# Optimization experiments

Hardware: AMD Instinct MI355X
Metric: run time of the kernel (lower is better)

Reference implementation:

```python
import jax, jax.numpy as jnp
import numpy as np

NDIM = 128
GDIM = 128
NUM_LAYERS = 2
B = 8192
IDX = 16          # nodes per graph
EPG = 32          # edges per graph
N = B * IDX       # total nodes = 131072
E = B * EPG       # total edges = 262144


def setup_inputs() -> dict:
    key = jax.random.key(0)
    ks = jax.random.split(key, 24)
    h = jax.random.normal(ks[0], (B, IDX, NDIM), dtype=jnp.float32)
    # edges constrained within each graph (flattened node indexing)
    gid = jnp.repeat(jnp.arange(B, dtype=jnp.int64), EPG)
    src = gid * IDX + jax.random.randint(ks[1], (E,), 0, IDX).astype(jnp.int64)
    dst = gid * IDX + jax.random.randint(ks[2], (E,), 0, IDX).astype(jnp.int64)
    edge_index = jnp.stack([src, dst], axis=0)
    s = 0.05
    inp = {
        'h': h,
        'edge_index': edge_index,
        'msg_W': jax.random.normal(ks[3], (NUM_LAYERS, 2 * NDIM, 2 * NDIM), jnp.float32) * s,
        'msg_b': jax.random.normal(ks[4], (NUM_LAYERS, 2 * NDIM), jnp.float32) * s,
        'msgr_W': jax.random.normal(ks[5], (NUM_LAYERS, 2 * NDIM, 2 * NDIM), jnp.float32) * s,
        'msgr_b': jax.random.normal(ks[6], (NUM_LAYERS, 2 * NDIM), jnp.float32) * s,
        'gru_Wih': jax.random.normal(ks[7], (NUM_LAYERS, 3 * NDIM, 2 * NDIM), jnp.float32) * s,
        'gru_Whh': jax.random.normal(ks[8], (NUM_LAYERS, 3 * NDIM, NDIM), jnp.float32) * s,
        'gru_bih': jax.random.normal(ks[9], (NUM_LAYERS, 3 * NDIM), jnp.float32) * s,
        'gru_bhh': jax.random.normal(ks[10], (NUM_LAYERS, 3 * NDIM), jnp.float32) * s,
        'fm_W': jax.random.normal(ks[11], (GDIM, NDIM), jnp.float32) * s,
        'fm_b': jax.random.normal(ks[12], (GDIM,), jnp.float32) * s,
        'gm_W': jax.random.normal(ks[13], (1, NDIM), jnp.float32) * s,
        'gm_b': jax.random.normal(ks[14], (1,), jnp.float32) * s,
        'fmi_W': jax.random.normal(ks[15], (GDIM, NDIM), jnp.float32) * s,
        'fmi_b': jax.random.normal(ks[16], (GDIM,), jnp.float32) * s,
        'gmi_W': jax.random.normal(ks[17], (1, NDIM), jnp.float32) * s,
        'gmi_b': jax.random.normal(ks[18], (1,), jnp.float32) * s,
    }
    return inp


def _gnn_forward(h, edge_index, msg_W, msg_b, msgr_W, msgr_b,
                 gru_Wih, gru_Whh, gru_bih, gru_bhh):
    # h: [N, ndim]; edge_index: [2, E] -> doubled with reversed edges -> [2, 2E]
    ei = jnp.concatenate([edge_index, edge_index[::-1]], axis=1)
    src, dst = ei[0], ei[1]
    e = edge_index.shape[1]
    n_nodes = h.shape[0]
    for l in range(NUM_LAYERS):
        # (eval mode: dropout p=0.0 is a no-op)
        h_j = h[src]                       # [2E, ndim]
        h_i = h[dst]                       # [2E, ndim]
        m = jnp.concatenate([h_j, h_i], axis=1)   # [2E, 2*ndim]
        m_fwd, m_rev = m[:e], m[e:]
        a = jnp.concatenate([
            m_fwd @ msg_W[l].T + msg_b[l],
            m_rev @ msgr_W[l].T + msgr_b[l],
        ], axis=0)                          # [2E, 2*ndim]
        aggr = jax.ops.segment_sum(a, dst, num_segments=n_nodes)  # [N, 2*ndim]
        # GRUCell(aggr, h): gate order r, z, n (torch convention)
        gi = aggr @ gru_Wih[l].T + gru_bih[l]   # [N, 3*ndim]
        gh = h @ gru_Whh[l].T + gru_bhh[l]      # [N, 3*ndim]
        gi_r, gi_z, gi_n = jnp.split(gi, 3, axis=1)
        gh_r, gh_z, gh_n = jnp.split(gh, 3, axis=1)
        r = jax.nn.sigmoid(gi_r + gh_r)
        z = jax.nn.sigmoid(gi_z + gh_z)
        n = jnp.tanh(gi_n + r * gh_n)
        h = n + z * (h - n)                 # (1-z)*n + z*h
    return h


def _graph_aggr(h, idx, f_W, f_b, g_W, g_b):
    # gated sum aggregation
    h_vG = h @ f_W.T + f_b                      # [N, gdim]
    g_vG = jax.nn.sigmoid(h @ g_W.T + g_b)      # [N, 1]
    out = (h_vG * g_vG).reshape(-1, idx, f_W.shape[0])
    return out.sum(axis=1)                      # [B, gdim]


def reference(h, edge_index, msg_W, msg_b, msgr_W, msgr_b,
              gru_Wih, gru_Whh, gru_bih, gru_bhh,
              fm_W, fm_b, gm_W, gm_b, fmi_W, fmi_b, gmi_W, gmi_b):
    idx = h.shape[1]
    hf = h.reshape(-1, NDIM)
    hf = _gnn_forward(hf, edge_index, msg_W, msg_b, msgr_W, msgr_b,
                      gru_Wih, gru_Whh, gru_bih, gru_bhh)
    h_G = _graph_aggr(hf, idx, fm_W, fm_b, gm_W, gm_b)
    h_G_init = _graph_aggr(hf, idx, fmi_W, fmi_b, gmi_W, gmi_b)
    return (hf.reshape(-1, idx, NDIM), h_G, h_G_init)
```

## Files before the change

kernel.cpp:

```cpp
#include <hip/hip_runtime.h>
#include <math.h>
#include <stdint.h>

#define NDIM 128
#define B_GRAPHS 8192
#define IDX 16
#define EPG 32
#define NN (B_GRAPHS*IDX)
#define NE (B_GRAPHS*EPG)

typedef short bf16x8 __attribute__((ext_vector_type(8)));
typedef float f32x4  __attribute__((ext_vector_type(4)));

__device__ inline unsigned short f2bf(float x) {
    union { float f; unsigned u; } v; v.f = x;
    unsigned r = v.u + 0x7fff + ((v.u >> 16) & 1);
    return (unsigned short)(r >> 16);
}
__device__ inline float bf2f(unsigned short b) {
    union { unsigned u; float f; } v; v.u = ((unsigned)b) << 16;
    return v.f;
}
__device__ inline float sigm(float x) { return 1.f/(1.f + __expf(-x)); }
__device__ inline float tanh_f(float x) {
    float ax = fabsf(x);
    float t  = __expf(-2.f*ax);
    float r  = (1.f - t)/(1.f + t);
    return copysignf(r, x);
}

#define GLOAD_LDS16(g, l) \
    __builtin_amdgcn_global_load_lds( \
        (const __attribute__((address_space(1))) unsigned int*)(g), \
        (__attribute__((address_space(3))) unsigned int*)(l), 16, 0, 0)

__global__ __launch_bounds__(256) void composemm_kernel(
    const float* __restrict__ msg_W, const float* __restrict__ msgr_W,
    const float* __restrict__ Wih, unsigned short* __restrict__ WB)
{
    int bid = blockIdx.x;
    int l  = bid / 48; int rem = bid - l*48;
    int ct = rem >> 3, kt = rem & 7;
    const int t = threadIdx.x;
    __shared__ float Ws[64][33];
    __shared__ float Ms[32][65];
    const float* wih    = Wih   + (size_t)l*384*256;
    const float* msgWl  = msg_W + (size_t)l*256*256;
    const float* msgrWl = msgr_W+ (size_t)l*256*256;
    float acc[4][4] = {};
    const int tr  = (t >> 4) * 4;
    const int tcc = (t & 15) * 4;
    for (int q0 = 0; q0 < 256; q0 += 32) {
#pragma unroll
        for (int i = 0; i < 8; i++) {
            int u = i*256 + t; int r = u >> 5, q = u & 31;
            Ws[r][q] = wih[(size_t)(ct*64 + r)*256 + q0 + q];
        }
#pragma unroll
        for (int i = 0; i < 8; i++) {
            int u = i*256 + t; int q = u >> 6, c = u & 63;
            int kk = kt*64 + c;
            int piece = kk >> 7;
            const float* M = (piece & 1) ? msgrWl : msgWl;
            int sc = (kk & 127) + ((piece >> 1) << 7);
            Ms[q][c] = M[(size_t)(q0 + q)*256 + sc];
        }
        __syncthreads();
#pragma unroll 8
        for (int q = 0; q < 32; q++) {
#pragma unroll
            for (int i2 = 0; i2 < 4; i2++) {
                float wv = Ws[tr + i2][q];
#pragma unroll
                for (int j2 = 0; j2 < 4; j2++)
                    acc[i2][j2] = fmaf(wv, Ms[q][tcc + j2], acc[i2][j2]);
            }
        }
        __syncthreads();
    }
#pragma unroll
    for (int i2 = 0; i2 < 4; i2++) {
        int cold = ct*64 + tr + i2;
        int cc = cold & 127, t2 = cold >> 7;
        int colp = ((cc >> 4) << 6) + (t2 << 4) + (cc & 15);
#pragma unroll
        for (int j2 = 0; j2 < 4; j2++) {
            int k = kt*64 + tcc + j2;
            WB[(size_t)l*512*640 + (size_t)colp*640 + k] = f2bf(acc[i2][j2]);
        }
    }
}

__global__ __launch_bounds__(256) void compose_kernel(
    const float* __restrict__ msg_W, const float* __restrict__ msgr_W,
    const float* __restrict__ Wih,   const float* __restrict__ Whh,
    const float* __restrict__ msg_b, const float* __restrict__ msgr_b,
    unsigned short* __restrict__ WB, float* __restrict__ c34)
{
    int idx = blockIdx.x*256 + threadIdx.x;
    const int TWB = 2*512*640;
    if (idx < TWB) {
        int l = idx / (512*640); int rem = idx - l*(512*640);
        int cold = rem / 640; int k = rem - cold*640;
        float val;
        if (k < 512) {
            if (cold < 384) return;
            val = 0.f;
        } else {
            int kk = k - 512;
            if (cold < 256)      val = Whh[l*384*128 + cold*128 + kk];
            else if (cold < 384) val = 0.f;
            else                 val = Whh[l*384*128 + (cold-128)*128 + kk];
        }
        int cc = cold & 127, t = cold >> 7;
        int colp = ((cc >> 4) << 6) + (t << 4) + (cc & 15);
        WB[l*512*640 + colp*640 + k] = f2bf(val);
    } else if (idx < TWB + 2*2*384) {
        int i2 = idx - TWB;
        int l = i2 / 768; int rem = i2 - l*768;
        int which = rem / 384; int r = rem - which*384;
        const float* wih = Wih + l*384*256 + r*256;
        const float* bb  = (which ? msgr_b : msg_b) + l*256;
        float acc = 0.f;
        for (int q = 0; q < 256; q++) acc = fmaf(wih[q], bb[q], acc);
        c34[l*768 + which*384 + r] = acc;
    }
}

__global__ __launch_bounds__(128) void init_kernel(
    const float* __restrict__ hin, const int* __restrict__ ei,
    unsigned short* __restrict__ A, float* __restrict__ indeg,
    float* __restrict__ outdeg, unsigned char* __restrict__ pack)
{
    int g = blockIdx.x, t = threadIdx.x;
    __shared__ float hb[16][128];
    __shared__ float sin_[16][128];
    __shared__ float sout_[16][128];
    __shared__ int sl[32], dl[32];
    __shared__ int cin[16], cout[16];
    __shared__ int flag64;
    int base = g*IDX;
    for (int r = 0; r < 16; r++) hb[r][t] = hin[(size_t)(base+r)*128 + t];
    for (int r = 0; r < 16; r++) { sin_[r][t] = 0.f; sout_[r][t] = 0.f; }
    if (t < 16) { cin[t] = 0; cout[t] = 0; }
    if (t == 0) {
        int orv = 0;
        for (int i = 1; i < 64; i += 2) orv |= ei[i];
        flag64 = (orv == 0);
    }
    __syncthreads();
    if (t < 32) {
        int e = g*EPG + t;
        int sv, dv;
        if (flag64) { sv = ei[2*e]; dv = ei[2*(NE + e)]; }
        else        { sv = ei[e];   dv = ei[NE + e];     }
        sl[t] = sv - base; dl[t] = dv - base;
        atomicAdd(&cout[sl[t]], 1); atomicAdd(&cin[dl[t]], 1);
        pack[g*32 + t] = (unsigned char)((sl[t] & 15) | ((dl[t] & 15) << 4));
    }
    __syncthreads();
    for (int e = 0; e < 32; e++) {
        sin_[dl[e]][t]  += hb[sl[e]][t];
        sout_[sl[e]][t] += hb[dl[e]][t];
    }
    __syncthreads();
    {
        size_t gbase = (size_t)base * 640;
#pragma unroll
        for (int i = 0; i < 10; i++) {
            int u = i*128 + t;
            int row = u / 80;
            int j   = u - row*80;
            int seg = j >> 4;
            int c0  = (j & 15) * 8;
            float vals[8];
            if (seg == 0) {
#pragma unroll
                for (int k2 = 0; k2 < 8; k2++) vals[k2] = sin_[row][c0+k2];
            } else if (seg == 1) {
#pragma unroll
                for (int k2 = 0; k2 < 8; k2++) vals[k2] = sout_[row][c0+k2];
            } else {
                float s = (seg == 2) ? (float)cin[row]
                        : (seg == 3) ? (float)cout[row] : 1.f;
#pragma unroll
                for (int k2 = 0; k2 < 8; k2++) vals[k2] = hb[row][c0+k2] * s;
            }
            bf16x8 w;
#pragma unroll
            for (int k2 = 0; k2 < 8; k2++) w[k2] = (short)f2bf(vals[k2]);
            *(bf16x8*)(A + gbase + (size_t)row*640 + seg*128 + c0) = w;
        }
    }
    if (t < 16) { indeg[base+t] = (float)cin[t]; outdeg[base+t] = (float)cout[t]; }
}

struct FSmem {
    unsigned short As[2][64*64];
    union {
        unsigned short Bs[2][384*32];
        unsigned short hnewB[64*128];
    } u;
    unsigned char csr[4][2][17];
    unsigned char adj[4][2][32];
    unsigned char offj[4][2][16];
    float gates[2][64];
};

#define MF(a,b,c) __builtin_amdgcn_mfma_f32_16x16x32_bf16((a),(b),(c),0,0,0)

#define CSTEP(BB, AB, E, J2) do {                                             \
    const unsigned short* Asb = sm.As[AB];                                    \
    const unsigned short* Bsb = sm.u.Bs[BB];                                  \
    bf16x8 bfv[3];                                                            \
    _Pragma("unroll")                                                         \
    for (int tt = 0; tt < 3; tt++) {                                          \
        int a0 = wid*48 + tt*16 + l15;                                        \
        bfv[tt] = *(const bf16x8*)(Bsb + a0*32 + (l4 ^ ((a0>>1)&3))*8);       \
    }                                                                         \
    bf16x8 afv[4];                                                            \
    _Pragma("unroll")                                                         \
    for (int mi = 0; mi < 4; mi++) {                                          \
        int row = mi*16 + l15;                                                \
        int slot = ((E)*4 + l4) ^ (row & 7);                                  \
        afv[mi] = *(const bf16x8*)(Asb + row*64 + slot*8);                    \
    }                                                                         \
    __builtin_amdgcn_s_setprio(1);                                            \
    _Pragma("unroll")                                                         \
    for (int mi = 0; mi < 4; mi++) {                                          \
        acc[mi][0]  = MF(afv[mi], bfv[0], acc[mi][0]);                        \
        acc[mi][1]  = MF(afv[mi], bfv[1], acc[mi][1]);                        \
        acc[mi][J2] = MF(afv[mi], bfv[2], acc[mi][J2]);                       \
    }                                                                         \
    __builtin_amdgcn_s_setprio(0);                                            \
} while (0)

#define WB0 asm volatile("s_waitcnt vmcnt(0)\n\ts_barrier" ::: "memory")
#define WB1 asm volatile("s_waitcnt vmcnt(1)\n\ts_barrier" ::: "memory")

template <bool FINAL>
__global__ __launch_bounds__(512, 4) void fused_kernel(
    unsigned short* __restrict__ A,
    const unsigned short* __restrict__ WBl,
    const unsigned char* __restrict__ pack,
    const float* __restrict__ c34l,
    const float* __restrict__ bihl, const float* __restrict__ bhhl,
    const float* __restrict__ gmW,  const float* __restrict__ gmb,
    const float* __restrict__ gmiW, const float* __restrict__ gmib,
    float* __restrict__ hf, float* __restrict__ P1, float* __restrict__ P2,
    float* __restrict__ sg)
{
    __shared__ FSmem sm;
    const int n0  = blockIdx.x * 64;
    const int g0  = blockIdx.x * 4;
    const int tid = threadIdx.x;
    const int lane = tid & 63, wid = tid >> 6;
    const int l15 = lane & 15, l4 = lane >> 4;

    const int arow = tid >> 3;
    const unsigned short* Abase =
        A + (size_t)(n0 + arow)*640 + (size_t)(((tid & 7) ^ (arow & 7)) * 8);
    int boffv[3], baddv[3];
#pragma unroll
    for (int i = 0; i < 3; i++) {
        int u = i*512 + tid;
        int a = u >> 2, s = u & 3;
        int grp = a / 48, rem = a - grp*48;
        int tt = rem >> 4, clo = rem & 15;
        boffv[i] = (grp*64 + tt*16 + clo)*640 + (s ^ ((a >> 1) & 3))*8;
        baddv[i] = (tt == 2) ? 16*640 : 0;
    }

    auto STAGE_A2 = [&](int p) {
        GLOAD_LDS16(Abase + p*64, sm.As[p & 1] + tid*8);
    };
    auto STAGE_B = [&](int kst) {
        unsigned short* dst = sm.u.Bs[kst & 1] + tid*8;
        const unsigned short* srcb = WBl + kst*32;
        if (kst < 16) {
#pragma unroll
            for (int i = 0; i < 3; i++)
                GLOAD_LDS16(srcb + boffv[i], dst + i*4096);
        } else {
#pragma unroll
            for (int i = 0; i < 3; i++)
                GLOAD_LDS16(srcb + boffv[i] + baddv[i], dst + i*4096);
        }
    };

    STAGE_B(0); STAGE_A2(0);
    if (tid < 8) {
        int gl = tid >> 1, dir = tid & 1;
        const unsigned char* pk = pack + (size_t)(g0 + gl)*32;
        unsigned char* C = sm.csr[gl][dir];
        for (int d = 0; d < 17; d++) C[d] = 0;
        for (int e = 0; e < 32; e++) {
            int p = pk[e];
            int key = dir ? (p & 15) : (p >> 4);
            C[key + 1]++;
        }
        for (int d = 0; d < 16; d++) { C[d+1] += C[d]; sm.offj[gl][dir][d] = C[d]; }
        for (int e = 0; e < 32; e++) {
            int p = pk[e];
            int key = dir ? (p & 15) : (p >> 4);
            int val = dir ? (p >> 4) : (p & 15);
            sm.adj[gl][dir][sm.offj[gl][dir][key]++] = val;
        }
    }

    f32x4 acc[4][4] = {};

    WB0;
    STAGE_B(1);  STAGE_A2(1); CSTEP(0, 0, 0, 2);
    WB1; STAGE_B(2);          CSTEP(1, 0, 1, 2);
    WB0; STAGE_B(3);  STAGE_A2(2); CSTEP(0, 1, 0, 2);
    WB1; STAGE_B(4);          CSTEP(1, 1, 1, 2);
    WB0; STAGE_B(5);  STAGE_A2(3); CSTEP(0, 0, 0, 2);
    WB1; STAGE_B(6);          CSTEP(1, 0, 1, 2);
    WB0; STAGE_B(7);  STAGE_A2(4); CSTEP(0, 1, 0, 2);
    WB1; STAGE_B(8);          CSTEP(1, 1, 1, 2);
    WB0; STAGE_B(9);  STAGE_A2(5); CSTEP(0, 0, 0, 2);
    WB1; STAGE_B(10);         CSTEP(1, 0, 1, 2);
    WB0; STAGE_B(11); STAGE_A2(6); CSTEP(0, 1, 0, 2);
    WB1; STAGE_B(12);         CSTEP(1, 1, 1, 2);
    WB0; STAGE_B(13); STAGE_A2(7); CSTEP(0, 0, 0, 2);
    WB1; STAGE_B(14);         CSTEP(1, 0, 1, 2);
    WB0; STAGE_B(15); STAGE_A2(8); CSTEP(0, 1, 0, 2);
    WB1; STAGE_B(16);         CSTEP(1, 1, 1, 2);
    WB0; STAGE_B(17); STAGE_A2(9); CSTEP(0, 0, 0, 3);
    WB1; STAGE_B(18);         CSTEP(1, 0, 1, 3);
    WB0; STAGE_B(19);         CSTEP(0, 1, 0, 3);
    WB0;                      CSTEP(1, 1, 1, 3);

    {
        const int chn = wid*16 + l15;
        const unsigned short* Ah = (chn < 64) ? sm.As[0] : sm.As[1];
        const int kl = chn & 63;
        const int klo = ((kl >> 3) << 3);
        float c3r = c34l[chn],     c3z = c34l[128+chn], c3n = c34l[256+chn];
        float c4r = c34l[384+chn], c4z = c34l[512+chn], c4n = c34l[640+chn];
        float br   = bihl[chn]     + bhhl[chn];
        float bz   = bihl[128+chn] + bhhl[128+chn];
        float bin_ = bihl[256+chn];
        float bhn_ = bhhl[256+chn];
#pragma unroll
        for (int mi = 0; mi < 4; mi++) {
#pragma unroll
            for (int q = 0; q < 4; q++) {
                int row = mi*16 + l4*4 + q;
                size_t v = (size_t)n0 + row;
                int gl = row >> 4, d = row & 15;
                float di  = (float)(sm.csr[gl][0][d+1] - sm.csr[gl][0][d]);
                float dof = (float)(sm.csr[gl][1][d+1] - sm.csr[gl][1][d]);
                float hold = bf2f(Ah[row*64 + (((kl>>3) ^ (row&7))<<3) + (kl&7)]);
                float rr = sigm(acc[mi][0][q] + di*c3r + dof*c4r + br);
                float zz = sigm(acc[mi][1][q] + di*c3z + dof*c4z + bz);
                float nn = tanh_f(acc[mi][2][q] + di*c3n + dof*c4n + bin_
                                  + rr*(acc[mi][3][q] + bhn_));
                float hv = nn + zz*(hold - nn);
                *(unsigned short*)((char*)sm.u.hnewB
                    + row*256 + ((((chn>>3) ^ (row&7))<<4) + ((chn&7)<<1))) = f2bf(hv);
                if (FINAL) hf[v*128 + chn] = hv;
            }
        }
    }
    __syncthreads();

    if (!FINAL) {
#pragma unroll
        for (int i = 0; i < 10; i++) {
            int u   = i*512 + tid;
            int seg = u >> 10;
            int row = (u >> 4) & 63;
            int c8  = u & 15;
            int gl = row >> 4, d = row & 15;
            float out8[8];
            if (seg < 2) {
#pragma unroll
                for (int k = 0; k < 8; k++) out8[k] = 0.f;
                int e0 = sm.csr[gl][seg][d], e1 = sm.csr[gl][seg][d+1];
                int rb = gl*16;
                for (int j = e0; j < e1; j++) {
                    int r2 = rb + sm.adj[gl][seg][j];
                    bf16x8 v8 = *(const bf16x8*)((const char*)sm.u.hnewB
                                 + r2*256 + ((c8 ^ (r2 & 7)) << 4));
#pragma unroll
                    for (int k = 0; k < 8; k++)
                        out8[k] += bf2f((unsigned short)v8[k]);
                }
            } else {
                bf16x8 v8 = *(const bf16x8*)((const char*)sm.u.hnewB
                             + row*256 + ((c8 ^ (row & 7)) << 4));
                float sc = 1.f;
                if (seg == 2)
                    sc = (float)(sm.csr[gl][0][d+1] - sm.csr[gl][0][d]);
                else if (seg == 3)
                    sc = (float)(sm.csr[gl][1][d+1] - sm.csr[gl][1][d]);
#pragma unroll
                for (int k = 0; k < 8; k++)
                    out8[k] = bf2f((unsigned short)v8[k]) * sc;
            }
            bf16x8 w;
#pragma unroll
            for (int k = 0; k < 8; k++) w[k] = (short)f2bf(out8[k]);
            *(bf16x8*)(A + (size_t)(n0 + row)*640 + seg*128 + c8*8) = w;
        }
    } else {
        if (tid < 64) {
            int row = tid;
            float a1 = 0.f, a2 = 0.f;
            for (int s = 0; s < 16; s++) {
                bf16x8 hv8 = *(const bf16x8*)((const char*)sm.u.hnewB
                              + row*256 + ((s ^ (row & 7)) << 4));
#pragma unroll
                for (int j = 0; j < 8; j++) {
                    float x = bf2f((unsigned short)hv8[j]);
                    int c = s*8 + j;
                    a1 = fmaf(gmW[c],  x, a1);
                    a2 = fmaf(gmiW[c], x, a2);
                }
            }
            sm.gates[0][row] = sigm(a1 + gmb[0]);
            sm.gates[1][row] = sigm(a2 + gmib[0]);
        }
        __syncthreads();
        int c = tid & 127, gq = tid >> 7;
        int rb = gq*16;
        float p1 = 0.f, p2 = 0.f;
        for (int r = 0; r < 16; r++) {
            int rr = rb + r;
            float x = bf2f(*(const unsigned short*)((const char*)sm.u.hnewB
                           + rr*256 + ((((c>>3) ^ (rr&7))<<4) + ((c&7)<<1))));
            p1 = fmaf(sm.gates[0][rr], x, p1);
            p2 = fmaf(sm.gates[1][rr], x, p2);
        }
        size_t g = g0 + gq;
        P1[g*128 + c] = p1;
        P2[g*128 + c] = p2;
        if (tid < 8) {
            int gl = tid >> 1, w = tid & 1;
            float s = 0.f;
            for (int r = 0; r < 16; r++) s += sm.gates[w][gl*16 + r];
            sg[(size_t)(g0 + gl)*2 + w] = s;
        }
    }
}

__global__ __launch_bounds__(256) void outgemm_kernel(
    const float* __restrict__ P1, const float* __restrict__ P2,
    const float* __restrict__ sg,
    const float* __restrict__ fm_W,  const float* __restrict__ fm_b,
    const float* __restrict__ fmi_W, const float* __restrict__ fmi_b,
    float* __restrict__ out1, float* __restrict__ out2)
{
    const int g0 = blockIdx.x * 32;
    const int t  = threadIdx.x;
    __shared__ float Ws[128][33];
    __shared__ float Ps[32][33];
    const int tc = t & 15, tg = t >> 4;

    for (int pass = 0; pass < 2; pass++) {
        const float* P  = pass ? P2 : P1;
        const float* W  = pass ? fmi_W : fm_W;
        const float* bb = pass ? fmi_b : fm_b;
        float acc[2][8] = {};
        for (int kc = 0; kc < 128; kc += 32) {
#pragma unroll
            for (int i = 0; i < 16; i++) {
                int u = i*256 + t; int r = u >> 5, k = u & 31;
                Ws[r][k] = W[(size_t)r*128 + kc + k];
            }
#pragma unroll
            for (int i = 0; i < 4; i++) {
                int u = i*256 + t; int r = u >> 5, k = u & 31;
                Ps[r][k] = P[(size_t)(g0 + r)*128 + kc + k];
            }
            __syncthreads();
#pragma unroll 8
            for (int k = 0; k < 32; k++) {
                float p0 = Ps[tg*2][k], p1v = Ps[tg*2+1][k];
#pragma unroll
                for (int j = 0; j < 8; j++) {
                    float w = Ws[tc*8+j][k];
                    acc[0][j] = fmaf(p0,  w, acc[0][j]);
                    acc[1][j] = fmaf(p1v, w, acc[1][j]);
                }
            }
            __syncthreads();
        }
        float* outp = pass ? out2 : out1;
#pragma unroll
        for (int i = 0; i < 2; i++) {
            int g = g0 + tg*2 + i;
            float sgv = sg[g*2 + pass];
#pragma unroll
            for (int j = 0; j < 8; j++) {
                int cc = tc*8 + j;
                outp[(size_t)g*128 + cc] = acc[i][j] + bb[cc]*sgv;
            }
        }
    }
}

extern "C" void kernel_launch(void* const* d_in, const int* in_sizes, int n_in,
                              void* d_out, int out_size, void* d_ws, size_t ws_size,
                              hipStream_t stream)
{
    const float* h     = (const float*)d_in[0];
    const int*   ei    = (const int*)d_in[1];
    const float* msgW  = (const float*)d_in[2];
    const float* msgb  = (const float*)d_in[3];
    const float* msgrW = (const float*)d_in[4];
    const float* msgrb = (const float*)d_in[5];
    const float* Wih   = (const float*)d_in[6];
    const float* Whh   = (const float*)d_in[7];
    const float* bih   = (const float*)d_in[8];
    const float* bhh   = (const float*)d_in[9];
    const float* fmW   = (const float*)d_in[10];
    const float* fmb   = (const float*)d_in[11];
    const float* gmW   = (const float*)d_in[12];
    const float* gmb   = (const float*)d_in[13];
    const float* fmiW  = (const float*)d_in[14];
    const float* fmib  = (const float*)d_in[15];
    const float* gmiW  = (const float*)d_in[16];
    const float* gmib  = (const float*)d_in[17];

    char* w = (char*)d_ws;
    unsigned short* A    = (unsigned short*)w;  w += (size_t)NN*640*2;
    unsigned short* WB   = (unsigned short*)w;  w += (size_t)2*512*640*2;
    float* c34   = (float*)w;                   w += (size_t)2*768*4;
    float* indeg = (float*)w;                   w += (size_t)NN*4;
    float* outdeg= (float*)w;                   w += (size_t)NN*4;
    unsigned char* pack = (unsigned char*)w;    w += (size_t)B_GRAPHS*32;
    float* P1    = (float*)w;                   w += (size_t)B_GRAPHS*128*4;
    float* P2    = (float*)w;                   w += (size_t)B_GRAPHS*128*4;
    float* sgb   = (float*)w;                   w += (size_t)B_GRAPHS*2*4;

    float* hf   = (float*)d_out;
    float* out1 = hf + (size_t)NN*128;
    float* out2 = out1 + (size_t)B_GRAPHS*128;

    composemm_kernel<<<96, 256, 0, stream>>>(msgW, msgrW, Wih, WB);
    int compose_items = 2*512*640 + 2*2*384;
    compose_kernel<<<(compose_items + 255)/256, 256, 0, stream>>>(
        msgW, msgrW, Wih, Whh, msgb, msgrb, WB, c34);

    init_kernel<<<B_GRAPHS, 128, 0, stream>>>(h, ei, A, indeg, outdeg, pack);

    fused_kernel<false><<<NN/64, 512, 0, stream>>>(
        A, WB, pack, c34, bih, bhh,
        gmW, gmb, gmiW, gmib, nullptr, nullptr, nullptr, nullptr);
    fused_kernel<true><<<NN/64, 512, 0, stream>>>(
        A, WB + (size_t)512*640, pack,
        c34 + 768, bih + 384, bhh + 384,
        gmW, gmb, gmiW, gmib, hf, P1, P2, sgb);

    outgemm_kernel<<<B_GRAPHS/32, 256, 0, stream>>>(
        P1, P2, sgb, fmW, fmb, fmiW, fmib, out1, out2);
}
```

Before: 412.3 us.

## Fuse both GNN layers into one kernel launch with block-local feature rewrite

Merges the two per-layer fused kernel launches into a single kernel that runs both layers back to back in each block. Each block rewrites its own A rows between layers, followed by a vmcnt wait and a barrier, and skips the separate CSR rebuild and launch. This works because edges stay inside a graph and a block owns whole graphs. It also drops the unused indeg/outdeg writes from init. The cost is that the second layer's A reads go back through global memory/L2 right after this block's own writes, which relies on intra-block visibility, and there are no cross-kernel boundaries left to hide latency.

After: 494.4 us. 19.9% more time.

```diff
diff --git a/kernel.cpp b/kernel.cpp
--- a/kernel.cpp
+++ b/kernel.cpp
@@ -129,8 +129,7 @@
 
 __global__ __launch_bounds__(128) void init_kernel(
     const float* __restrict__ hin, const int* __restrict__ ei,
-    unsigned short* __restrict__ A, float* __restrict__ indeg,
-    float* __restrict__ outdeg, unsigned char* __restrict__ pack)
+    unsigned short* __restrict__ A, unsigned char* __restrict__ pack)
 {
     int g = blockIdx.x, t = threadIdx.x;
     __shared__ float hb[16][128];
@@ -192,7 +191,6 @@
             *(bf16x8*)(A + gbase + (size_t)row*640 + seg*128 + c0) = w;
         }
     }
-    if (t < 16) { indeg[base+t] = (float)cin[t]; outdeg[base+t] = (float)cout[t]; }
 }
 
 struct FSmem {
@@ -238,13 +236,12 @@
 #define WB0 asm volatile("s_waitcnt vmcnt(0)\n\ts_barrier" ::: "memory")
 #define WB1 asm volatile("s_waitcnt vmcnt(1)\n\ts_barrier" ::: "memory")
 
-template <bool FINAL>
-__global__ __launch_bounds__(512, 4) void fused_kernel(
+__global__ __launch_bounds__(512, 4) void gnn_kernel(
     unsigned short* __restrict__ A,
-    const unsigned short* __restrict__ WBl,
+    const unsigned short* __restrict__ WB,
     const unsigned char* __restrict__ pack,
-    const float* __restrict__ c34l,
-    const float* __restrict__ bihl, const float* __restrict__ bhhl,
+    const float* __restrict__ c34,
+    const float* __restrict__ bih, const float* __restrict__ bhh,
     const float* __restrict__ gmW,  const float* __restrict__ gmb,
     const float* __restrict__ gmiW, const float* __restrict__ gmib,
     float* __restrict__ hf, float* __restrict__ P1, float* __restrict__ P2,
@@ -258,7 +255,7 @@
     const int l15 = lane & 15, l4 = lane >> 4;
 
     const int arow = tid >> 3;
-    const unsigned short* Abase =
+    unsigned short* Abase =
         A + (size_t)(n0 + arow)*640 + (size_t)(((tid & 7) ^ (arow & 7)) * 8);
     int boffv[3], baddv[3];
 #pragma unroll
@@ -271,24 +268,6 @@
         baddv[i] = (tt == 2) ? 16*640 : 0;
     }
 
-    auto STAGE_A2 = [&](int p) {
-        GLOAD_LDS16(Abase + p*64, sm.As[p & 1] + tid*8);
-    };
-    auto STAGE_B = [&](int kst) {
-        unsigned short* dst = sm.u.Bs[kst & 1] + tid*8;
-        const unsigned short* srcb = WBl + kst*32;
-        if (kst < 16) {
-#pragma unroll
-            for (int i = 0; i < 3; i++)
-                GLOAD_LDS16(srcb + boffv[i], dst + i*4096);
-        } else {
-#pragma unroll
-            for (int i = 0; i < 3; i++)
-                GLOAD_LDS16(srcb + boffv[i] + baddv[i], dst + i*4096);
-        }
-    };
-
-    STAGE_B(0); STAGE_A2(0);
     if (tid < 8) {
         int gl = tid >> 1, dir = tid & 1;
         const unsigned char* pk = pack + (size_t)(g0 + gl)*32;
@@ -308,122 +287,149 @@
         }
     }
 
-    f32x4 acc[4][4] = {};
-
-    WB0;
-    STAGE_B(1);  STAGE_A2(1); CSTEP(0, 0, 0, 2);
-    WB1; STAGE_B(2);          CSTEP(1, 0, 1, 2);
-    WB0; STAGE_B(3);  STAGE_A2(2); CSTEP(0, 1, 0, 2);
-    WB1; STAGE_B(4);          CSTEP(1, 1, 1, 2);
-    WB0; STAGE_B(5);  STAGE_A2(3); CSTEP(0, 0, 0, 2);
-    WB1; STAGE_B(6);          CSTEP(1, 0, 1, 2);
-    WB0; STAGE_B(7);  STAGE_A2(4); CSTEP(0, 1, 0, 2);
-    WB1; STAGE_B(8);          CSTEP(1, 1, 1, 2);
-    WB0; STAGE_B(9);  STAGE_A2(5); CSTEP(0, 0, 0, 2);
-    WB1; STAGE_B(10);         CSTEP(1, 0, 1, 2);
-    WB0; STAGE_B(11); STAGE_A2(6); CSTEP(0, 1, 0, 2);
-    WB1; STAGE_B(12);         CSTEP(1, 1, 1, 2);
-    WB0; STAGE_B(13); STAGE_A2(7); CSTEP(0, 0, 0, 2);
-    WB1; STAGE_B(14);         CSTEP(1, 0, 1, 2);
-    WB0; STAGE_B(15); STAGE_A2(8); CSTEP(0, 1, 0, 2);
-    WB1; STAGE_B(16);         CSTEP(1, 1, 1, 2);
-    WB0; STAGE_B(17); STAGE_A2(9); CSTEP(0, 0, 0, 3);
-    WB1; STAGE_B(18);         CSTEP(1, 0, 1, 3);
-    WB0; STAGE_B(19);         CSTEP(0, 1, 0, 3);
-    WB0;                      CSTEP(1, 1, 1, 3);
-
+    auto do_layer = [&](const unsigned short* WBl, const float* c34l,
+                        const float* bihl, const float* bhhl, bool fin) {
+        auto STAGE_A2 = [&](int p) {
+            GLOAD_LDS16(Abase + p*64, sm.As[p & 1] + tid*8);
+        };
+        auto STAGE_B = [&](int kst) {
+            unsigned short* dst = sm.u.Bs[kst & 1] + tid*8;
+            const unsigned short* srcb = WBl + kst*32;
+            if (kst < 16) {
+#pragma unroll
+                for (int i = 0; i < 3; i++)
+                    GLOAD_LDS16(srcb + boffv[i], dst + i*4096);
+            } else {
+#pragma unroll
+                for (int i = 0; i < 3; i++)
+                    GLOAD_LDS16(srcb + boffv[i] + baddv[i], dst + i*4096);
+            }
+        };
+
+        f32x4 acc[4][4] = {};
+
+        STAGE_B(0); STAGE_A2(0);
+        WB0;
+        STAGE_B(1);  STAGE_A2(1); CSTEP(0, 0, 0, 2);
+        WB1; STAGE_B(2);          CSTEP(1, 0, 1, 2);
+        WB0; STAGE_B(3);  STAGE_A2(2); CSTEP(0, 1, 0, 2);
+        WB1; STAGE_B(4);          CSTEP(1, 1, 1, 2);
+        WB0; STAGE_B(5);  STAGE_A2(3); CSTEP(0, 0, 0, 2);
+        WB1; STAGE_B(6);          CSTEP(1, 0, 1, 2);
+        WB0; STAGE_B(7);  STAGE_A2(4); CSTEP(0, 1, 0, 2);
+        WB1; STAGE_B(8);          CSTEP(1, 1, 1, 2);
+        WB0; STAGE_B(9);  STAGE_A2(5); CSTEP(0, 0, 0, 2);
+        WB1; STAGE_B(10);         CSTEP(1, 0, 1, 2);
+        WB0; STAGE_B(11); STAGE_A2(6); CSTEP(0, 1, 0, 2);
+        WB1; STAGE_B(12);         CSTEP(1, 1, 1, 2);
+        WB0; STAGE_B(13); STAGE_A2(7); CSTEP(0, 0, 0, 2);
+        WB1; STAGE_B(14);         CSTEP(1, 0, 1, 2);
+        WB0; STAGE_B(15); STAGE_A2(8); CSTEP(0, 1, 0, 2);
+        WB1; STAGE_B(16);         CSTEP(1, 1, 1, 2);
+        WB0; STAGE_B(17); STAGE_A2(9); CSTEP(0, 0, 0, 3);
+        WB1; STAGE_B(18);         CSTEP(1, 0, 1, 3);
+        WB0; STAGE_B(19);         CSTEP(0, 1, 0, 3);
+        WB0;                      CSTEP(1, 1, 1, 3);
+
+        {
+            const int chn = wid*16 + l15;
+            const unsigned short* Ah = (chn < 64) ? sm.As[0] : sm.As[1];
+            const int kl = chn & 63;
+            float c3r = c34l[chn],     c3z = c34l[128+chn], c3n = c34l[256+chn];
+            float c4r = c34l[384+chn], c4z = c34l[512+chn], c4n = c34l[640+chn];
+            float br   = bihl[chn]     + bhhl[chn];
+            float bz   = bihl[128+chn] + bhhl[128+chn];
+            float bin_ = bihl[256+chn];
+            float bhn_ = bhhl[256+chn];
+#pragma unroll
+            for (int mi = 0; mi < 4; mi++) {
+#pragma unroll
+                for (int q = 0; q < 4; q++) {
+                    int row = mi*16 + l4*4 + q;
+                    size_t v = (size_t)n0 + row;
+                    int gl = row >> 4, d = row & 15;
+                    float di  = (float)(sm.csr[gl][0][d+1] - sm.csr[gl][0][d]);
+                    float dof = (float)(sm.csr[gl][1][d+1] - sm.csr[gl][1][d]);
+                    float hold = bf2f(Ah[row*64 + (((kl>>3) ^ (row&7))<<3) + (kl&7)]);
+                    float rr = sigm(acc[mi][0][q] + di*c3r + dof*c4r + br);
+                    float zz = sigm(acc[mi][1][q] + di*c3z + dof*c4z + bz);
+                    float nn = tanh_f(acc[mi][2][q] + di*c3n + dof*c4n + bin_
+                                      + rr*(acc[mi][3][q] + bhn_));
+                    float hv = nn + zz*(hold - nn);
+                    *(unsigned short*)((char*)sm.u.hnewB
+                        + row*256 + ((((chn>>3) ^ (row&7))<<4) + ((chn&7)<<1))) = f2bf(hv);
+                    if (fin) hf[v*128 + chn] = hv;
+                }
+            }
+        }
+        __syncthreads();
+
+        if (!fin) {
+#pragma unroll
+            for (int i = 0; i < 10; i++) {
+                int u   = i*512 + tid;
+                int seg = u >> 10;
+                int row = (u >> 4) & 63;
+                int c8  = u & 15;
+                int gl = row >> 4, d = row & 15;
+                float out8[8];
+                if (seg < 2) {
+#pragma unroll
+                    for (int k = 0; k < 8; k++) out8[k] = 0.f;
+                    int e0 = sm.csr[gl][seg][d], e1 = sm.csr[gl][seg][d+1];
+                    int rb = gl*16;
+                    for (int j = e0; j < e1; j++) {
+                        int r2 = rb + sm.adj[gl][seg][j];
+                        bf16x8 v8 = *(const bf16x8*)((const char*)sm.u.hnewB
+                                     + r2*256 + ((c8 ^ (r2 & 7)) << 4));
+#pragma unroll
+                        for (int k = 0; k < 8; k++)
+                            out8[k] += bf2f((unsigned short)v8[k]);
+                    }
+                } else {
+                    bf16x8 v8 = *(const bf16x8*)((const char*)sm.u.hnewB
+                                 + row*256 + ((c8 ^ (row & 7)) << 4));
+                    float sc = 1.f;
+                    if (seg == 2)
+                        sc = (float)(sm.csr[gl][0][d+1] - sm.csr[gl][0][d]);
+                    else if (seg == 3)
+                        sc = (float)(sm.csr[gl][1][d+1] - sm.csr[gl][1][d]);
+#pragma unroll
+                    for (int k = 0; k < 8; k++)
+                        out8[k] = bf2f((unsigned short)v8[k]) * sc;
+                }
+                bf16x8 w;
+#pragma unroll
+                for (int k = 0; k < 8; k++) w[k] = (short)f2bf(out8[k]);
+                *(bf16x8*)(A + (size_t)(n0 + row)*640 + seg*128 + c8*8) = w;
+            }
+            asm volatile("s_waitcnt vmcnt(0)" ::: "memory");
+            __syncthreads();
+        }
+    };
+
+    do_layer(WB,                    c34,       bih,       bhh,       false);
+    do_layer(WB + (size_t)512*640,  c34 + 768, bih + 384, bhh + 384, true);
+
+    if (tid < 64) {
+        int row = tid;
+        float a1 = 0.f, a2 = 0.f;
+        for (int s = 0; s < 16; s++) {
+            bf16x8 hv8 = *(const bf16x8*)((const char*)sm.u.hnewB
+                          + row*256 + ((s ^ (row & 7)) << 4));
+#pragma unroll
+            for (int j = 0; j < 8; j++) {
+                float x = bf2f((unsigned short)hv8[j]);
+                int c = s*8 + j;
+                a1 = fmaf(gmW[c],  x, a1);
+                a2 = fmaf(gmiW[c], x, a2);
+            }
+        }
+        sm.gates[0][row] = sigm(a1 + gmb[0]);
+        sm.gates[1][row] = sigm(a2 + gmib[0]);
+    }
+    __syncthreads();
     {
-        const int chn = wid*16 + l15;
-        const unsigned short* Ah = (chn < 64) ? sm.As[0] : sm.As[1];
-        const int kl = chn & 63;
-        const int klo = ((kl >> 3) << 3);
-        float c3r = c34l[chn],     c3z = c34l[128+chn], c3n = c34l[256+chn];
-        float c4r = c34l[384+chn], c4z = c34l[512+chn], c4n = c34l[640+chn];
-        float br   = bihl[chn]     + bhhl[chn];
-        float bz   = bihl[128+chn] + bhhl[128+chn];
-        float bin_ = bihl[256+chn];
-        float bhn_ = bhhl[256+chn];
-#pragma unroll
-        for (int mi = 0; mi < 4; mi++) {
-#pragma unroll
-            for (int q = 0; q < 4; q++) {
-                int row = mi*16 + l4*4 + q;
-                size_t v = (size_t)n0 + row;
-                int gl = row >> 4, d = row & 15;
-                float di  = (float)(sm.csr[gl][0][d+1] - sm.csr[gl][0][d]);
-                float dof = (float)(sm.csr[gl][1][d+1] - sm.csr[gl][1][d]);
-                float hold = bf2f(Ah[row*64 + (((kl>>3) ^ (row&7))<<3) + (kl&7)]);
-                float rr = sigm(acc[mi][0][q] + di*c3r + dof*c4r + br);
-                float zz = sigm(acc[mi][1][q] + di*c3z + dof*c4z + bz);
-                float nn = tanh_f(acc[mi][2][q] + di*c3n + dof*c4n + bin_
-                                  + rr*(acc[mi][3][q] + bhn_));
-                float hv = nn + zz*(hold - nn);
-                *(unsigned short*)((char*)sm.u.hnewB
-                    + row*256 + ((((chn>>3) ^ (row&7))<<4) + ((chn&7)<<1))) = f2bf(hv);
-                if (FINAL) hf[v*128 + chn] = hv;
-            }
-        }
-    }
-    __syncthreads();
-
-    if (!FINAL) {
-#pragma unroll
-        for (int i = 0; i < 10; i++) {
-            int u   = i*512 + tid;
-            int seg = u >> 10;
-            int row = (u >> 4) & 63;
-            int c8  = u & 15;
-            int gl = row >> 4, d = row & 15;
-            float out8[8];
-            if (seg < 2) {
-#pragma unroll
-                for (int k = 0; k < 8; k++) out8[k] = 0.f;
-                int e0 = sm.csr[gl][seg][d], e1 = sm.csr[gl][seg][d+1];
-                int rb = gl*16;
-                for (int j = e0; j < e1; j++) {
-                    int r2 = rb + sm.adj[gl][seg][j];
-                    bf16x8 v8 = *(const bf16x8*)((const char*)sm.u.hnewB
-                                 + r2*256 + ((c8 ^ (r2 & 7)) << 4));
-#pragma unroll
-                    for (int k = 0; k < 8; k++)
-                        out8[k] += bf2f((unsigned short)v8[k]);
-                }
-            } else {
-                bf16x8 v8 = *(const bf16x8*)((const char*)sm.u.hnewB
-                             + row*256 + ((c8 ^ (row & 7)) << 4));
-                float sc = 1.f;
-                if (seg == 2)
-                    sc = (float)(sm.csr[gl][0][d+1] - sm.csr[gl][0][d]);
-                else if (seg == 3)
-                    sc = (float)(sm.csr[gl][1][d+1] - sm.csr[gl][1][d]);
-#pragma unroll
-                for (int k = 0; k < 8; k++)
-                    out8[k] = bf2f((unsigned short)v8[k]) * sc;
-            }
-            bf16x8 w;
-#pragma unroll
-            for (int k = 0; k < 8; k++) w[k] = (short)f2bf(out8[k]);
-            *(bf16x8*)(A + (size_t)(n0 + row)*640 + seg*128 + c8*8) = w;
-        }
-    } else {
-        if (tid < 64) {
-            int row = tid;
-            float a1 = 0.f, a2 = 0.f;
-            for (int s = 0; s < 16; s++) {
-                bf16x8 hv8 = *(const bf16x8*)((const char*)sm.u.hnewB
-                              + row*256 + ((s ^ (row & 7)) << 4));
-#pragma unroll
-                for (int j = 0; j < 8; j++) {
-                    float x = bf2f((unsigned short)hv8[j]);
-                    int c = s*8 + j;
-                    a1 = fmaf(gmW[c],  x, a1);
-                    a2 = fmaf(gmiW[c], x, a2);
-                }
-            }
-            sm.gates[0][row] = sigm(a1 + gmb[0]);
-            sm.gates[1][row] = sigm(a2 + gmib[0]);
-        }
-        __syncthreads();
         int c = tid & 127, gq = tid >> 7;
         int rb = gq*16;
         float p1 = 0.f, p2 = 0.f;
@@ -437,12 +443,12 @@
         size_t g = g0 + gq;
         P1[g*128 + c] = p1;
         P2[g*128 + c] = p2;
-        if (tid < 8) {
-            int gl = tid >> 1, w = tid & 1;
-            float s = 0.f;
-            for (int r = 0; r < 16; r++) s += sm.gates[w][gl*16 + r];
-            sg[(size_t)(g0 + gl)*2 + w] = s;
-        }
+    }
+    if (tid < 8) {
+        int gl = tid >> 1, w = tid & 1;
+        float s = 0.f;
+        for (int r = 0; r < 16; r++) s += sm.gates[w][gl*16 + r];
+        sg[(size_t)(g0 + gl)*2 + w] = s;
     }
 }
 
@@ -529,8 +535,6 @@
     unsigned short* A    = (unsigned short*)w;  w += (size_t)NN*640*2;
     unsigned short* WB   = (unsigned short*)w;  w += (size_t)2*512*640*2;
     float* c34   = (float*)w;                   w += (size_t)2*768*4;
-    float* indeg = (float*)w;                   w += (size_t)NN*4;
-    float* outdeg= (float*)w;                   w += (size_t)NN*4;
     unsigned char* pack = (unsigned char*)w;    w += (size_t)B_GRAPHS*32;
     float* P1    = (float*)w;                   w += (size_t)B_GRAPHS*128*4;
     float* P2    = (float*)w;                   w += (size_t)B_GRAPHS*128*4;
@@ -545,14 +549,10 @@
     compose_kernel<<<(compose_items + 255)/256, 256, 0, stream>>>(
         msgW, msgrW, Wih, Whh, msgb, msgrb, WB, c34);
 
-    init_kernel<<<B_GRAPHS, 128, 0, stream>>>(h, ei, A, indeg, outdeg, pack);
-
-    fused_kernel<false><<<NN/64, 512, 0, stream>>>(
+    init_kernel<<<B_GRAPHS, 128, 0, stream>>>(h, ei, A, pack);
+
+    gnn_kernel<<<NN/64, 512, 0, stream>>>(
         A, WB, pack, c34, bih, bhh,
-        gmW, gmb, gmiW, gmib, nullptr, nullptr, nullptr, nullptr);
-    fused_kernel<true><<<NN/64, 512, 0, stream>>>(
-        A, WB + (size_t)512*640, pack,
-        c34 + 768, bih + 384, bhh + 384,
         gmW, gmb, gmiW, gmib, hf, P1, P2, sgb);
 
     outgemm_kernel<<<B_GRAPHS/32, 256, 0, stream>>>(
```
